# Performance work log

Measured on AMD Instinct MI355X. Metric: run time of the kernel, lower is better.

Reference implementation:

```python
import jax, jax.numpy as jnp
import numpy as np

B, T = 256, 50
N_ITEMS = 100000
EMB = 256      # embedding
KBD = 128      # KBembedding == MN_dims
HID = 256      # layers[0] == layers[-1]
OUT = 256      # out_dim
NF = 10        # MN_nfactors == n_r


def setup_inputs() -> dict:
    key = jax.random.key(0)
    ks = jax.random.split(key, 18)
    s = 0.05
    return {
        "X": jax.random.randint(ks[0], (B, T), 0, N_ITEMS),
        "E": jax.random.normal(ks[1], (N_ITEMS, EMB), jnp.float32) * s,
        "KBE": jax.random.normal(ks[2], (N_ITEMS, KBD), jnp.float32) * s,
        "r_matrix": jax.random.normal(ks[3], (NF, KBD), jnp.float32) * s,
        "W_ih": jax.random.normal(ks[4], (3 * HID, EMB), jnp.float32) * s,
        "W_hh": jax.random.normal(ks[5], (3 * HID, HID), jnp.float32) * s,
        "b_ih": jnp.zeros((3 * HID,), jnp.float32),
        "b_hh": jnp.zeros((3 * HID,), jnp.float32),
        "MNu_W": jax.random.normal(ks[6], (KBD, HID), jnp.float32) * s,
        "MNu_b": jnp.zeros((KBD,), jnp.float32),
        "MNu2_W": jax.random.normal(ks[7], (HID, KBD + HID), jnp.float32) * s,
        "MNu2_b": jnp.zeros((HID,), jnp.float32),
        "MNea_W": jax.random.normal(ks[8], (KBD, KBD), jnp.float32) * s,
        "MNea_b": jnp.zeros((KBD,), jnp.float32),
        "mlp1_W": jax.random.normal(ks[9], (OUT, HID), jnp.float32) * s,
        "mlp1_b": jnp.zeros((OUT,), jnp.float32),
        "mlp2_W": jax.random.normal(ks[10], (OUT, EMB + KBD), jnp.float32) * s,
        "mlp2_b": jnp.zeros((OUT,), jnp.float32),
    }


def _gru_cell(x, h, W_ih, W_hh, b_ih, b_hh):
    # PyTorch GRUCell: gates stacked [r, z, n] along dim 0 of weights
    gi = x @ W_ih.T + b_ih
    gh = h @ W_hh.T + b_hh
    ir, iz, inn = jnp.split(gi, 3, axis=-1)
    hr, hz, hn = jnp.split(gh, 3, axis=-1)
    r = jax.nn.sigmoid(ir + hr)
    z = jax.nn.sigmoid(iz + hz)
    n = jnp.tanh(inn + r * hn)
    return (1.0 - z) * n + z * h


def reference(X, E, KBE, r_matrix, W_ih, W_hh, b_ih, b_hh,
              MNu_W, MNu_b, MNu2_W, MNu2_b, MNea_W, MNea_b,
              mlp1_W, mlp1_b, mlp2_W, mlp2_b):
    Bv, Tv = X.shape
    Em = E.at[0].set(0.0)     # mask row 0 of E
    KBm = KBE.at[0].set(0.0)  # mask row 0 of KBE
    Sx = Em[X]                # (B, T, EMB)
    KBItem = KBm[X]           # (B, T, KBD)

    def step(carry, xs):
        h, MN, y_sum = carry
        x_t, kb_t = xs                      # (B, EMB), (B, KBD)
        h = _gru_cell(x_t, h, W_ih, W_hh, b_ih, b_hh)
        y = h                                # dropout p=0 -> identity
        # gated memory write
        EA = jnp.tanh(kb_t @ MNea_W.T + MNea_b)          # (B, KBD)
        EA = EA[:, None, :] + r_matrix                    # (B, NF, KBD)
        gate = jax.nn.sigmoid(jnp.sum(MN * EA, axis=-1, keepdims=True))  # (B, NF, 1)
        MN = MN * (1.0 - gate) + EA * gate
        # attention read
        U = jnp.tanh(y @ MNu_W.T + MNu_b)                 # (B, KBD)
        AW = jax.nn.softmax(U @ r_matrix.T, axis=1)       # (B, NF)
        AC = jnp.einsum('bfd,bf->bd', MN, AW)             # (B, KBD)
        Ut = jnp.tanh(jnp.concatenate([y, AC], axis=-1) @ MNu2_W.T + MNu2_b)  # (B, HID)
        y_out = jnp.tanh(Ut @ mlp1_W.T + mlp1_b)          # (B, OUT)
        return (h, MN, y_sum + y_out), None

    init = (jnp.zeros((Bv, HID), Sx.dtype),
            jnp.zeros((Bv, NF, KBD), Sx.dtype),
            jnp.zeros((Bv, OUT), Sx.dtype))
    xs = (jnp.swapaxes(Sx, 0, 1), jnp.swapaxes(KBItem, 0, 1))  # (T, B, *)
    (h, MN, y_sum), _ = jax.lax.scan(step, init, xs)
    y = y_sum / Tv

    MergeE = jnp.concatenate([E, KBE], axis=1).at[0].set(0.0)  # (N, EMB+KBD)
    Sy = jnp.tanh(MergeE @ mlp2_W.T + mlp2_b)                  # (N, OUT)
    scores = jax.nn.log_softmax(y @ Sy.T, axis=1)              # (B, N)
    return scores, y
```

## Files before the change

kernel.cpp:

```cpp
#include <hip/hip_runtime.h>

typedef _Float16 f16;
typedef _Float16 f16x2 __attribute__((ext_vector_type(2)));
typedef _Float16 f16x8 __attribute__((ext_vector_type(8)));
typedef float f32x4 __attribute__((ext_vector_type(4)));
typedef int i32x4 __attribute__((ext_vector_type(4)));

#define MFMA16(a,b,c) __builtin_amdgcn_mfma_f32_16x16x32_f16(a,b,c,0,0,0)

#define NITEMS 100000
#define NBLK4  1563

#define OFF_WIH   0u
#define OFF_WHH   393216u
#define OFF_MNU   786432u
#define OFF_MNU2  851968u
#define OFF_MNEA  1048576u
#define OFF_MLP1  1081344u
#define OFF_MLP2  1212416u
#define OFF_WHHD  1409024u
#define OFF_GI    1802240u
#define OFF_TV    21463040u
#define OFF_MN    24739840u
#define OFF_YALL  57507840u
#define OFF_SY    64061440u
#define OFF_Y16   115261440u
#define OFF_PMAX  115392512u
#define OFF_PSUM  117030912u
#define OFF_LSE   118669312u

__device__ __forceinline__ float sigm(float x) { return 1.f / (1.f + __expf(-x)); }
__device__ __forceinline__ float tanh_fast(float x) {
  return 1.f - 2.f / (1.f + __expf(2.f * x));
}
__device__ __forceinline__ float fdot2(f16x2 a, f16x2 b, float c) {
#if defined(__has_builtin)
#if __has_builtin(__builtin_amdgcn_fdot2)
  return __builtin_amdgcn_fdot2(a, b, c, false);
#else
  return fmaf((float)a[1], (float)b[1], fmaf((float)a[0], (float)b[0], c));
#endif
#else
  return fmaf((float)a[1], (float)b[1], fmaf((float)a[0], (float)b[0], c));
#endif
}

__global__ __launch_bounds__(256) void k_pack(
    const float* s0, const float* s1, const float* s2, const float* s3,
    const float* s4, const float* s5, const float* s6, f16* base)
{
  int fid = blockIdx.x * 256 + threadIdx.x;
  if (fid >= 88064) {
    int g = fid - 88064;
    const float* sp = s1 + (size_t)g * 8;
    f16* dst = (f16*)((char*)base + OFF_WHHD);
    f16x8 v;
    #pragma unroll
    for (int j = 0; j < 8; j++) v[j] = (f16)sp[j];
    *(f16x8*)(dst + (size_t)g * 8) = v;
    return;
  }
  const float* src; f16* dst; int K, f;
  if (fid < 24576)      { src = s0; dst = base;          K = 256; f = fid; }
  else if (fid < 49152) { src = s1; dst = base + 196608; K = 256; f = fid - 24576; }
  else if (fid < 53248) { src = s2; dst = base + 393216; K = 256; f = fid - 49152; }
  else if (fid < 65536) { src = s3; dst = base + 425984; K = 384; f = fid - 53248; }
  else if (fid < 67584) { src = s4; dst = base + 524288; K = 128; f = fid - 65536; }
  else if (fid < 75776) { src = s5; dst = base + 540672; K = 256; f = fid - 67584; }
  else                  { src = s6; dst = base + 606208; K = 384; f = fid - 75776; }
  int lane = f & 63, t2 = f >> 6, KS = K >> 5;
  int ks = t2 % KS, nt = t2 / KS;
  int row = nt * 16 + (lane & 15), col = ks * 32 + ((lane >> 4) << 3);
  const float* sp = src + (size_t)row * K + col;
  f16x8 v;
  #pragma unroll
  for (int j = 0; j < 8; j++) v[j] = (f16)sp[j];
  *(f16x8*)(dst + (size_t)f * 8) = v;
}

__global__ __launch_bounds__(512) void k_prep(
    const int* __restrict__ X, const float* __restrict__ E,
    const f16* __restrict__ Wih_p, const float* __restrict__ bih,
    const float* __restrict__ bhh, f16* __restrict__ gi,
    const float* __restrict__ KBE, const f16* __restrict__ Wea_p,
    const float* __restrict__ bea, f16* __restrict__ tv,
    const f16* __restrict__ mlp2_p, const float* __restrict__ mlp2b, f16* __restrict__ Sy)
{
  __shared__ __align__(16) char smem[66048];
  f16 (*At)[264] = (f16(*)[264])smem;
  f16* Lg2 = (f16*)(smem + 16896);
  int tid = threadIdx.x;
  int w = tid >> 6, lane = tid & 63, lr = lane & 15, lg = lane >> 4;
  if (blockIdx.x < 400) {
    int r0g = blockIdx.x * 32;
    int t = r0g >> 8;
    {
      int r = tid >> 4, c = (tid & 15) * 16;
      int b = (r0g + r) & 255;
      int item = X[b * 50 + t];
      if (item == 0) {
        #pragma unroll
        for (int j = 0; j < 16; j++) At[r][c + j] = (f16)0.f;
      } else {
        const float4* sp = (const float4*)(E + (size_t)item * 256 + c);
        #pragma unroll
        for (int q = 0; q < 4; q++) {
          float4 v = sp[q];
          At[r][c + q*4 + 0] = (f16)v.x; At[r][c + q*4 + 1] = (f16)v.y;
          At[r][c + q*4 + 2] = (f16)v.z; At[r][c + q*4 + 3] = (f16)v.w;
        }
      }
    }
    __syncthreads();
    f32x4 acc[2][6] = {};
    for (int ks = 0; ks < 8; ks++) {
      f16x8 a0 = *(const f16x8*)(&At[lr][ks * 32 + lg * 8]);
      f16x8 a1 = *(const f16x8*)(&At[16 + lr][ks * 32 + lg * 8]);
      #pragma unroll
      for (int j = 0; j < 6; j++) {
        int nt = w * 6 + j;
        f16x8 bf = *(const f16x8*)(Wih_p + ((size_t)((nt * 8 + ks) * 64 + lane) << 3));
        acc[0][j] = MFMA16(a0, bf, acc[0][j]);
        acc[1][j] = MFMA16(a1, bf, acc[1][j]);
      }
    }
    #pragma unroll
    for (int j = 0; j < 6; j++) {
      int col = (w * 6 + j) * 16 + lr;
      float bias = bih[col] + (col < 512 ? bhh[col] : 0.f);
      #pragma unroll
      for (int mt = 0; mt < 2; mt++)
        #pragma unroll
        for (int rr = 0; rr < 4; rr++)
          Lg2[(mt * 16 + lg * 4 + rr) * 768 + col] = (f16)(acc[mt][j][rr] + bias);
    }
    __syncthreads();
    f16* dst = gi + (size_t)r0g * 768;
    #pragma unroll
    for (int q = 0; q < 6; q++) {
      int u = q * 512 + tid;
      *(f16x8*)(dst + u * 8) = *(const f16x8*)(Lg2 + u * 8);
    }
  } else if (blockIdx.x < 800) {
    int r0 = (blockIdx.x - 400) * 32;
    int t = r0 >> 8;
    {
      int r = tid >> 4, c = (tid & 15) * 8;
      int b = (r0 + r) & 255;
      int item = X[b * 50 + t];
      if (item == 0) {
        #pragma unroll
        for (int j = 0; j < 8; j++) At[r][c + j] = (f16)0.f;
      } else {
        const float4* sp = (const float4*)(KBE + (size_t)item * 128 + c);
        #pragma unroll
        for (int q = 0; q < 2; q++) {
          float4 v = sp[q];
          At[r][c + q*4 + 0] = (f16)v.x; At[r][c + q*4 + 1] = (f16)v.y;
          At[r][c + q*4 + 2] = (f16)v.z; At[r][c + q*4 + 3] = (f16)v.w;
        }
      }
    }
    __syncthreads();
    f32x4 acc[2] = {};
    for (int ks = 0; ks < 4; ks++) {
      f16x8 a0 = *(const f16x8*)(&At[lr][ks * 32 + lg * 8]);
      f16x8 a1 = *(const f16x8*)(&At[16 + lr][ks * 32 + lg * 8]);
      f16x8 bf = *(const f16x8*)(Wea_p + ((size_t)((w * 4 + ks) * 64 + lane) << 3));
      acc[0] = MFMA16(a0, bf, acc[0]);
      acc[1] = MFMA16(a1, bf, acc[1]);
    }
    f16* tvs = Lg2;
    int col = w * 16 + lr;
    float bias = bea[col];
    #pragma unroll
    for (int mt = 0; mt < 2; mt++)
      #pragma unroll
      for (int rr = 0; rr < 4; rr++)
        tvs[(mt * 16 + lg * 4 + rr) * 128 + col] = (f16)tanh_fast(acc[mt][rr] + bias);
    __syncthreads();
    {
      int row = tid >> 4, c = (tid & 15) * 8;
      *(f16x8*)(tv + (size_t)(r0 + row) * 128 + c) = *(const f16x8*)(tvs + row * 128 + c);
    }
  } else {
    f16* A2 = (f16*)smem;
    int i0 = (blockIdx.x - 800) * 32;
    {
      int r = tid >> 4;
      int item = i0 + r;
      f16* rowp = A2 + r * 392;
      int cE = (tid & 15) * 16, cK = (tid & 15) * 8;
      if (item == 0) {
        #pragma unroll
        for (int j = 0; j < 16; j++) rowp[cE + j] = (f16)0.f;
        #pragma unroll
        for (int j = 0; j < 8; j++) rowp[256 + cK + j] = (f16)0.f;
      } else {
        const float4* sp = (const float4*)(E + (size_t)item * 256 + cE);
        #pragma unroll
        for (int q = 0; q < 4; q++) {
          float4 v = sp[q];
          rowp[cE + q*4 + 0] = (f16)v.x; rowp[cE + q*4 + 1] = (f16)v.y;
          rowp[cE + q*4 + 2] = (f16)v.z; rowp[cE + q*4 + 3] = (f16)v.w;
        }
        const float4* kp = (const float4*)(KBE + (size_t)item * 128 + cK);
        #pragma unroll
        for (int q = 0; q < 2; q++) {
          float4 v = kp[q];
          rowp[256 + cK + q*4 + 0] = (f16)v.x; rowp[256 + cK + q*4 + 1] = (f16)v.y;
          rowp[256 + cK + q*4 + 2] = (f16)v.z; rowp[256 + cK + q*4 + 3] = (f16)v.w;
        }
      }
    }
    __syncthreads();
    int mt = w & 1, nq = w >> 1;
    f32x4 acc[4] = {};
    for (int ks = 0; ks < 12; ks++) {
      f16x8 a = *(const f16x8*)(&A2[(mt * 16 + lr) * 392 + ks * 32 + lg * 8]);
      #pragma unroll
      for (int j = 0; j < 4; j++) {
        int nt = nq * 4 + j;
        f16x8 bf = *(const f16x8*)(mlp2_p + ((size_t)((nt * 12 + ks) * 64 + lane) << 3));
        acc[j] = MFMA16(a, bf, acc[j]);
      }
    }
    #pragma unroll
    for (int j = 0; j < 4; j++) {
      int col = (nq * 4 + j) * 16 + lr;
      float bias = mlp2b[col];
      #pragma unroll
      for (int rr = 0; rr < 4; rr++) {
        int item = i0 + mt * 16 + lg * 4 + rr;
        Sy[(size_t)item * 256 + col] = (f16)tanh_fast(acc[j][rr] + bias);
      }
    }
  }
}

__global__ __launch_bounds__(1024) void k_scan(
    const f16* __restrict__ Whh_d, const float* __restrict__ bhh,
    const f16* __restrict__ gi, f16* __restrict__ y_all,
    const f16* __restrict__ tv, const float* __restrict__ Rm, f16* __restrict__ MN)
{
  int tid = threadIdx.x, w = tid >> 6, l = tid & 63;
  if (blockIdx.x < 256) {
    __shared__ __align__(16) f16 hbuf[4 * 72];
    __shared__ float ghbuf[768];
    int b = blockIdx.x;
    int chunk = l >> 4, cl = l & 15;
    i32x4 Wv[3][8];
    #pragma unroll
    for (int j = 0; j < 3; j++) {
      int col = w * 48 + j * 16 + cl;
      const f16* wp = Whh_d + (size_t)col * 256 + chunk * 64;
      #pragma unroll
      for (int m = 0; m < 8; m++)
        Wv[j][m] = *(const i32x4*)(wp + m * 8);
    }
    float hprev = 0.f, bN = 0.f;
    f16 gr = (f16)0.f, gz = (f16)0.f, gn = (f16)0.f;
    if (tid < 256) {
      hbuf[(tid >> 6) * 72 + (tid & 63)] = (f16)0.f;
      bN = bhh[512 + tid];
      const f16* g0 = gi + (size_t)b * 768 + tid;
      gr = g0[0]; gz = g0[256]; gn = g0[512];
    }
    __syncthreads();
    const f16* hb = hbuf + chunk * 72;
    for (int t = 0; t < 50; t++) {
      float s0 = 0.f, s1 = 0.f, s2 = 0.f;
      #pragma unroll
      for (int m = 0; m < 8; m++) {
        i32x4 hw = *(const i32x4*)(hb + m * 8);
        #pragma unroll
        for (int p = 0; p < 4; p++) {
          f16x2 hp = __builtin_bit_cast(f16x2, hw[p]);
          s0 = fdot2(hp, __builtin_bit_cast(f16x2, Wv[0][m][p]), s0);
          s1 = fdot2(hp, __builtin_bit_cast(f16x2, Wv[1][m][p]), s1);
          s2 = fdot2(hp, __builtin_bit_cast(f16x2, Wv[2][m][p]), s2);
        }
      }
      s0 += __shfl_xor(s0, 16); s0 += __shfl_xor(s0, 32);
      s1 += __shfl_xor(s1, 16); s1 += __shfl_xor(s1, 32);
      s2 += __shfl_xor(s2, 16); s2 += __shfl_xor(s2, 32);
      if (l < 16) {
        ghbuf[w * 48 + l]      = s0;
        ghbuf[w * 48 + 16 + l] = s1;
        ghbuf[w * 48 + 32 + l] = s2;
      }
      __syncthreads();
      if (tid < 256) {
        int c = tid;
        float rg = sigm((float)gr + ghbuf[c]);
        float zg = sigm((float)gz + ghbuf[256 + c]);
        float ng = tanh_fast((float)gn + rg * (ghbuf[512 + c] + bN));
        float hv = ng + zg * (hprev - ng);
        hprev = hv;
        hbuf[(c >> 6) * 72 + (c & 63)] = (f16)hv;
        y_all[((size_t)t * 256 + b) * 256 + c] = (f16)hv;
        if (t < 49) {
          const f16* gN = gi + ((size_t)(t + 1) * 256 + b) * 768 + c;
          gr = gN[0]; gz = gN[256]; gn = gN[512];
        }
      }
      __syncthreads();
    }
  } else {
    int lane = l;
    int pair = (blockIdx.x - 256) * 16 + w;
    int b = pair / 10, f = pair - (pair / 10) * 10;
    float r0_ = Rm[f * 128 + lane], r1_ = Rm[f * 128 + 64 + lane];
    float mn0 = 0.f, mn1 = 0.f;
    float c0 = (float)tv[(size_t)b * 128 + lane];
    float c1 = (float)tv[(size_t)b * 128 + 64 + lane];
    for (int t = 0; t < 50; t++) {
      float ea0 = c0 + r0_;
      float ea1 = c1 + r1_;
      if (t < 49) {
        size_t nb = ((size_t)(t + 1) * 256 + b) * 128;
        c0 = (float)tv[nb + lane];
        c1 = (float)tv[nb + 64 + lane];
      }
      float p = mn0 * ea0 + mn1 * ea1;
      #pragma unroll
      for (int off = 32; off > 0; off >>= 1) p += __shfl_xor(p, off);
      float g = sigm(p);
      mn0 += (ea0 - mn0) * g;
      mn1 += (ea1 - mn1) * g;
      size_t mb = (((size_t)t * 256 + b) * 10 + f) * 128;
      MN[mb + lane] = (f16)mn0;
      MN[mb + 64 + lane] = (f16)mn1;
    }
  }
}

__global__ __launch_bounds__(512) void k_uacut(
    const f16* __restrict__ y_all, const f16* __restrict__ MNu_p,
    const float* __restrict__ MNub, const float* __restrict__ Rm,
    const f16* __restrict__ MN,
    const f16* __restrict__ MNu2_p, const float* __restrict__ MNu2b,
    const f16* __restrict__ mlp1_p, const float* __restrict__ mlp1b,
    float* __restrict__ ypart)
{
  __shared__ __align__(16) char smem[25088];
  int tid = threadIdx.x, w = tid >> 6, lane = tid & 63, lr = lane & 15, lg = lane >> 4;
  f16   (*Aty)[264] = (f16(*)[264])smem;
  float (*Uf)[136]  = (float(*)[136])(smem + 8448);
  f16   (*Utl)[264] = (f16(*)[264])(smem + 8448);
  float (*Lg)[10]   = (float(*)[10])(smem + 17152);
  float (*Aw)[10]   = (float(*)[10])(smem + 17792);
  f16   (*ACs)[136] = (f16(*)[136])(smem + 18432);
  int r0 = blockIdx.x * 16;
  {
    int r = tid >> 5, c = (tid & 31) * 8;
    f16x8 v = *(const f16x8*)(y_all + (size_t)(r0 + r) * 256 + c);
    *(f16x8*)(&Aty[r][c]) = v;
  }
  __syncthreads();
  {
    f32x4 acc = {};
    for (int ks = 0; ks < 8; ks++) {
      f16x8 a = *(const f16x8*)(&Aty[lr][ks * 32 + lg * 8]);
      f16x8 bf = *(const f16x8*)(MNu_p + ((size_t)((w * 8 + ks) * 64 + lane) << 3));
      acc = MFMA16(a, bf, acc);
    }
    int col = w * 16 + lr;
    float bias = MNub[col];
    #pragma unroll
    for (int rr = 0; rr < 4; rr++)
      Uf[lg * 4 + rr][col] = tanh_fast(acc[rr] + bias);
  }
  __syncthreads();
  if (tid < 160) {
    int row = tid / 10, f = tid - (tid / 10) * 10;
    float s = 0.f;
    for (int d = 0; d < 128; d++) s += Uf[row][d] * Rm[f * 128 + d];
    Lg[row][f] = s;
  }
  __syncthreads();
  if (tid < 16) {
    float m = -1e30f;
    #pragma unroll
    for (int f = 0; f < 10; f++) m = fmaxf(m, Lg[tid][f]);
    float e[10], s = 0.f;
    #pragma unroll
    for (int f = 0; f < 10; f++) { e[f] = __expf(Lg[tid][f] - m); s += e[f]; }
    float inv = 1.f / s;
    #pragma unroll
    for (int f = 0; f < 10; f++) Aw[tid][f] = e[f] * inv;
  }
  __syncthreads();
  if (tid < 256) {
    int row = tid >> 4, d0 = (tid & 15) * 8;
    float a[8] = {0,0,0,0,0,0,0,0};
    for (int f = 0; f < 10; f++) {
      float wgt = Aw[row][f];
      f16x8 mv = *(const f16x8*)(MN + (((size_t)(r0 + row)) * 10 + f) * 128 + d0);
      #pragma unroll
      for (int q = 0; q < 8; q++) a[q] += wgt * (float)mv[q];
    }
    f16x8 o;
    #pragma unroll
    for (int q = 0; q < 8; q++) o[q] = (f16)a[q];
    *(f16x8*)(&ACs[row][d0]) = o;
  }
  __syncthreads();
  {
    f32x4 acc[2] = {};
    for (int ks = 0; ks < 12; ks++) {
      f16x8 a = (ks < 8)
        ? *(const f16x8*)(&Aty[lr][ks * 32 + lg * 8])
        : *(const f16x8*)(&ACs[lr][(ks - 8) * 32 + lg * 8]);
      #pragma unroll
      for (int j = 0; j < 2; j++) {
        f16x8 bf = *(const f16x8*)(MNu2_p + ((size_t)(((w * 2 + j) * 12 + ks) * 64 + lane) << 3));
        acc[j] = MFMA16(a, bf, acc[j]);
      }
    }
    __syncthreads();
    #pragma unroll
    for (int j = 0; j < 2; j++) {
      int col = (w * 2 + j) * 16 + lr;
      float bias = MNu2b[col];
      #pragma unroll
      for (int rr = 0; rr < 4; rr++)
        Utl[lg * 4 + rr][col] = (f16)tanh_fast(acc[j][rr] + bias);
    }
  }
  __syncthreads();
  {
    f32x4 acc2[2] = {};
    for (int ks = 0; ks < 8; ks++) {
      f16x8 a = *(const f16x8*)(&Utl[lr][ks * 32 + lg * 8]);
      #pragma unroll
      for (int j = 0; j < 2; j++) {
        f16x8 bf = *(const f16x8*)(mlp1_p + ((size_t)(((w * 2 + j) * 8 + ks) * 64 + lane) << 3));
        acc2[j] = MFMA16(a, bf, acc2[j]);
      }
    }
    #pragma unroll
    for (int j = 0; j < 2; j++) {
      int col = (w * 2 + j) * 16 + lr;
      float bias = mlp1b[col];
      #pragma unroll
      for (int rr = 0; rr < 4; rr++) {
        int row = r0 + lg * 4 + rr;
        ypart[(size_t)row * 256 + col] = tanh_fast(acc2[j][rr] + bias);
      }
    }
  }
}

__global__ __launch_bounds__(256) void k_yfin(
    const float* __restrict__ ypart, float* __restrict__ outy, f16* __restrict__ y16)
{
  int b = blockIdx.x, c = threadIdx.x;
  float s = 0.f;
  for (int t = 0; t < 50; t++) s += ypart[((size_t)t * 256 + b) * 256 + c];
  float v = s * (1.0f / 50.0f);
  outy[b * 256 + c] = v;
  y16[b * 256 + c] = (f16)v;
}

__global__ __launch_bounds__(512) void k_score0(
    const f16* __restrict__ y16, const f16* __restrict__ Sy,
    float* __restrict__ pmax, float* __restrict__ psum)
{
  __shared__ float pm[512], ps[512];
  int tid = threadIdx.x, w = tid >> 6, lane = tid & 63, lr = lane & 15, lg = lane >> 4;
  int i0 = blockIdx.x * 64;
  int mtb = (w >> 1) * 4, ntb = (w & 1) * 2;
  f32x4 acc[4][2] = {};
  for (int ks = 0; ks < 8; ks++) {
    f16x8 a[4];
    #pragma unroll
    for (int i = 0; i < 4; i++)
      a[i] = *(const f16x8*)(y16 + ((size_t)((mtb + i) * 16 + lr)) * 256 + ks * 32 + lg * 8);
    #pragma unroll
    for (int j = 0; j < 2; j++) {
      int item = i0 + (ntb + j) * 16 + lr;
      int ic = item < NITEMS ? item : (NITEMS - 1);
      f16x8 bv = *(const f16x8*)(Sy + (size_t)ic * 256 + ks * 32 + lg * 8);
      #pragma unroll
      for (int i = 0; i < 4; i++) acc[i][j] = MFMA16(a[i], bv, acc[i][j]);
    }
  }
  {
    int item0 = i0 + ntb * 16 + lr, item1 = item0 + 16;
    bool v0 = item0 < NITEMS, v1 = item1 < NITEMS;
    #pragma unroll
    for (int i = 0; i < 4; i++)
      #pragma unroll
      for (int rr = 0; rr < 4; rr++) {
        float x0 = v0 ? acc[i][0][rr] : -1e30f;
        float x1 = v1 ? acc[i][1][rr] : -1e30f;
        float m = fmaxf(x0, x1);
        m = fmaxf(m, __shfl_xor(m, 1)); m = fmaxf(m, __shfl_xor(m, 2));
        m = fmaxf(m, __shfl_xor(m, 4)); m = fmaxf(m, __shfl_xor(m, 8));
        float s = (v0 ? __expf(x0 - m) : 0.f) + (v1 ? __expf(x1 - m) : 0.f);
        s += __shfl_xor(s, 1); s += __shfl_xor(s, 2);
        s += __shfl_xor(s, 4); s += __shfl_xor(s, 8);
        if (lr == 0) {
          int row = (mtb + i) * 16 + lg * 4 + rr;
          pm[(w & 1) * 256 + row] = m;
          ps[(w & 1) * 256 + row] = s;
        }
      }
  }
  __syncthreads();
  if (tid < 256) {
    float m0 = pm[tid], m1 = pm[256 + tid];
    float s0 = ps[tid], s1 = ps[256 + tid];
    float M = fmaxf(m0, m1);
    float S = s0 * __expf(m0 - M) + s1 * __expf(m1 - M);
    pmax[(size_t)tid * 1600 + blockIdx.x] = M;
    psum[(size_t)tid * 1600 + blockIdx.x] = S;
  }
}

__global__ __launch_bounds__(256) void k_lse(
    const float* __restrict__ pmax, const float* __restrict__ psum, float* __restrict__ lse)
{
  int b = blockIdx.x, tid = threadIdx.x;
  __shared__ float red[256];
  float m = -1e30f;
  for (int i = tid; i < NBLK4; i += 256) m = fmaxf(m, pmax[(size_t)b * 1600 + i]);
  red[tid] = m; __syncthreads();
  for (int s = 128; s > 0; s >>= 1) {
    if (tid < s) red[tid] = fmaxf(red[tid], red[tid + s]);
    __syncthreads();
  }
  float M = red[0]; __syncthreads();
  float s = 0.f;
  for (int i = tid; i < NBLK4; i += 256)
    s += psum[(size_t)b * 1600 + i] * __expf(pmax[(size_t)b * 1600 + i] - M);
  red[tid] = s; __syncthreads();
  for (int q = 128; q > 0; q >>= 1) {
    if (tid < q) red[tid] += red[tid + q];
    __syncthreads();
  }
  if (tid == 0) lse[b] = M + logf(red[0]);
}

__global__ __launch_bounds__(512) void k_scores1(
    const f16* __restrict__ y16, const f16* __restrict__ Sy,
    const float* __restrict__ lse, float* __restrict__ out)
{
  __shared__ float lse_s[256];
  int tid = threadIdx.x, w = tid >> 6, lane = tid & 63, lr = lane & 15, lg = lane >> 4;
  if (tid < 256) lse_s[tid] = lse[tid];
  int i0 = blockIdx.x * 64;
  int mtb = (w >> 1) * 4, ntb = (w & 1) * 2;
  f32x4 acc[4][2] = {};
  for (int ks = 0; ks < 8; ks++) {
    f16x8 a[4];
    #pragma unroll
    for (int i = 0; i < 4; i++)
      a[i] = *(const f16x8*)(y16 + ((size_t)((mtb + i) * 16 + lr)) * 256 + ks * 32 + lg * 8);
    #pragma unroll
    for (int j = 0; j < 2; j++) {
      int item = i0 + (ntb + j) * 16 + lr;
      int ic = item < NITEMS ? item : (NITEMS - 1);
      f16x8 bv = *(const f16x8*)(Sy + (size_t)ic * 256 + ks * 32 + lg * 8);
      #pragma unroll
      for (int i = 0; i < 4; i++) acc[i][j] = MFMA16(a[i], bv, acc[i][j]);
    }
  }
  __syncthreads();
  #pragma unroll
  for (int i = 0; i < 4; i++)
    #pragma unroll
    for (int j = 0; j < 2; j++) {
      int c = i0 + (ntb + j) * 16 + lr;
      if (c < NITEMS) {
        #pragma unroll
        for (int rr = 0; rr < 4; rr++) {
          int row = (mtb + i) * 16 + lg * 4 + rr;
          out[(size_t)row * NITEMS + c] = acc[i][j][rr] - lse_s[row];
        }
      }
    }
}

extern "C" void kernel_launch(void* const* d_in, const int* in_sizes, int n_in,
                              void* d_out, int out_size, void* d_ws, size_t ws_size,
                              hipStream_t stream) {
  (void)in_sizes; (void)n_in; (void)out_size; (void)ws_size;
  const int*   X     = (const int*)d_in[0];
  const float* E     = (const float*)d_in[1];
  const float* KBE   = (const float*)d_in[2];
  const float* Rm    = (const float*)d_in[3];
  const float* Wih   = (const float*)d_in[4];
  const float* Whh   = (const float*)d_in[5];
  const float* bih   = (const float*)d_in[6];
  const float* bhh   = (const float*)d_in[7];
  const float* MNuW  = (const float*)d_in[8];
  const float* MNub  = (const float*)d_in[9];
  const float* MNu2W = (const float*)d_in[10];
  const float* MNu2b = (const float*)d_in[11];
  const float* MNeaW = (const float*)d_in[12];
  const float* MNeab = (const float*)d_in[13];
  const float* mlp1W = (const float*)d_in[14];
  const float* mlp1b = (const float*)d_in[15];
  const float* mlp2W = (const float*)d_in[16];
  const float* mlp2b = (const float*)d_in[17];

  char* ws = (char*)d_ws;
  f16*   Wih_p  = (f16*)(ws + OFF_WIH);
  f16*   MNu_p  = (f16*)(ws + OFF_MNU);
  f16*   MNu2_p = (f16*)(ws + OFF_MNU2);
  f16*   Wea_p  = (f16*)(ws + OFF_MNEA);
  f16*   mlp1_p = (f16*)(ws + OFF_MLP1);
  f16*   mlp2_p = (f16*)(ws + OFF_MLP2);
  f16*   Whh_d  = (f16*)(ws + OFF_WHHD);
  f16*   gi     = (f16*)(ws + OFF_GI);
  f16*   tv     = (f16*)(ws + OFF_TV);
  f16*   MN     = (f16*)(ws + OFF_MN);
  f16*   y_all  = (f16*)(ws + OFF_YALL);
  f16*   Sy     = (f16*)(ws + OFF_SY);
  float* ypart  = (float*)(ws + OFF_GI);
  f16*   y16    = (f16*)(ws + OFF_Y16);
  float* pmax   = (float*)(ws + OFF_PMAX);
  float* psum   = (float*)(ws + OFF_PSUM);
  float* lse    = (float*)(ws + OFF_LSE);
  float* outf   = (float*)d_out;

  k_pack<<<440, 256, 0, stream>>>(Wih, Whh, MNuW, MNu2W, MNeaW, mlp1W, mlp2W, (f16*)ws);
  k_prep<<<3925, 512, 0, stream>>>(X, E, Wih_p, bih, bhh, gi, KBE, Wea_p, MNeab, tv,
                                   mlp2_p, mlp2b, Sy);
  k_scan<<<416, 1024, 0, stream>>>(Whh_d, bhh, gi, y_all, tv, Rm, MN);
  k_uacut<<<800, 512, 0, stream>>>(y_all, MNu_p, MNub, Rm, MN,
                                   MNu2_p, MNu2b, mlp1_p, mlp1b, ypart);
  k_yfin<<<256, 256, 0, stream>>>(ypart, outf + 25600000, y16);
  k_score0<<<NBLK4, 512, 0, stream>>>(y16, Sy, pmax, psum);
  k_lse<<<256, 256, 0, stream>>>(pmax, psum, lse);
  k_scores1<<<NBLK4, 512, 0, stream>>>(y16, Sy, lse, outf);
}
```

Measured before the change: 398.6 us.

## Move item projection (Sy) into the scan kernel to overlap with the recurrence

The Sy = tanh(MergeE @ mlp2_W.T) computation over all 100k items moves out of the prep kernel and into extra blocks of the scan launch, rewritten for 1024-thread blocks. The 256 serial GRU blocks and 160 memory-network blocks run alongside 3125 independent GEMM blocks, so the latency-bound recurrence can be hidden behind the bandwidth-heavy item projection. The risk is that the GEMM blocks compete with the latency-critical scan blocks for CU resources. The scan blocks also hit the launch_bounds(1024) register limit while holding weights in registers.

```diff
diff --git a/kernel.cpp b/kernel.cpp
--- a/kernel.cpp
+++ b/kernel.cpp
@@ -83,8 +83,7 @@
     const f16* __restrict__ Wih_p, const float* __restrict__ bih,
     const float* __restrict__ bhh, f16* __restrict__ gi,
     const float* __restrict__ KBE, const f16* __restrict__ Wea_p,
-    const float* __restrict__ bea, f16* __restrict__ tv,
-    const f16* __restrict__ mlp2_p, const float* __restrict__ mlp2b, f16* __restrict__ Sy)
+    const float* __restrict__ bea, f16* __restrict__ tv)
 {
   __shared__ __align__(16) char smem[66048];
   f16 (*At)[264] = (f16(*)[264])smem;
@@ -141,7 +140,7 @@
       int u = q * 512 + tid;
       *(f16x8*)(dst + u * 8) = *(const f16x8*)(Lg2 + u * 8);
     }
-  } else if (blockIdx.x < 800) {
+  } else {
     int r0 = (blockIdx.x - 400) * 32;
     int t = r0 >> 8;
     {
@@ -183,70 +182,21 @@
       int row = tid >> 4, c = (tid & 15) * 8;
       *(f16x8*)(tv + (size_t)(r0 + row) * 128 + c) = *(const f16x8*)(tvs + row * 128 + c);
     }
-  } else {
-    f16* A2 = (f16*)smem;
-    int i0 = (blockIdx.x - 800) * 32;
-    {
-      int r = tid >> 4;
-      int item = i0 + r;
-      f16* rowp = A2 + r * 392;
-      int cE = (tid & 15) * 16, cK = (tid & 15) * 8;
-      if (item == 0) {
-        #pragma unroll
-        for (int j = 0; j < 16; j++) rowp[cE + j] = (f16)0.f;
-        #pragma unroll
-        for (int j = 0; j < 8; j++) rowp[256 + cK + j] = (f16)0.f;
-      } else {
-        const float4* sp = (const float4*)(E + (size_t)item * 256 + cE);
-        #pragma unroll
-        for (int q = 0; q < 4; q++) {
-          float4 v = sp[q];
-          rowp[cE + q*4 + 0] = (f16)v.x; rowp[cE + q*4 + 1] = (f16)v.y;
-          rowp[cE + q*4 + 2] = (f16)v.z; rowp[cE + q*4 + 3] = (f16)v.w;
-        }
-        const float4* kp = (const float4*)(KBE + (size_t)item * 128 + cK);
-        #pragma unroll
-        for (int q = 0; q < 2; q++) {
-          float4 v = kp[q];
-          rowp[256 + cK + q*4 + 0] = (f16)v.x; rowp[256 + cK + q*4 + 1] = (f16)v.y;
-          rowp[256 + cK + q*4 + 2] = (f16)v.z; rowp[256 + cK + q*4 + 3] = (f16)v.w;
-        }
-      }
-    }
-    __syncthreads();
-    int mt = w & 1, nq = w >> 1;
-    f32x4 acc[4] = {};
-    for (int ks = 0; ks < 12; ks++) {
-      f16x8 a = *(const f16x8*)(&A2[(mt * 16 + lr) * 392 + ks * 32 + lg * 8]);
-      #pragma unroll
-      for (int j = 0; j < 4; j++) {
-        int nt = nq * 4 + j;
-        f16x8 bf = *(const f16x8*)(mlp2_p + ((size_t)((nt * 12 + ks) * 64 + lane) << 3));
-        acc[j] = MFMA16(a, bf, acc[j]);
-      }
-    }
-    #pragma unroll
-    for (int j = 0; j < 4; j++) {
-      int col = (nq * 4 + j) * 16 + lr;
-      float bias = mlp2b[col];
-      #pragma unroll
-      for (int rr = 0; rr < 4; rr++) {
-        int item = i0 + mt * 16 + lg * 4 + rr;
-        Sy[(size_t)item * 256 + col] = (f16)tanh_fast(acc[j][rr] + bias);
-      }
-    }
-  }
-}
-
-__global__ __launch_bounds__(1024) void k_scan(
+  }
+}
+
+__global__ __launch_bounds__(1024) void k_fused2(
     const f16* __restrict__ Whh_d, const float* __restrict__ bhh,
     const f16* __restrict__ gi, f16* __restrict__ y_all,
-    const f16* __restrict__ tv, const float* __restrict__ Rm, f16* __restrict__ MN)
-{
+    const f16* __restrict__ tv, const float* __restrict__ Rm, f16* __restrict__ MN,
+    const float* __restrict__ E, const float* __restrict__ KBE,
+    const f16* __restrict__ mlp2_p, const float* __restrict__ mlp2b, f16* __restrict__ Sy)
+{
+  __shared__ __align__(16) char smem[25088];
   int tid = threadIdx.x, w = tid >> 6, l = tid & 63;
   if (blockIdx.x < 256) {
-    __shared__ __align__(16) f16 hbuf[4 * 72];
-    __shared__ float ghbuf[768];
+    f16* hbuf = (f16*)smem;
+    float* ghbuf = (float*)(smem + 1024);
     int b = blockIdx.x;
     int chunk = l >> 4, cl = l & 15;
     i32x4 Wv[3][8];
@@ -306,7 +256,7 @@
       }
       __syncthreads();
     }
-  } else {
+  } else if (blockIdx.x < 416) {
     int lane = l;
     int pair = (blockIdx.x - 256) * 16 + w;
     int b = pair / 10, f = pair - (pair / 10) * 10;
@@ -331,6 +281,58 @@
       size_t mb = (((size_t)t * 256 + b) * 10 + f) * 128;
       MN[mb + lane] = (f16)mn0;
       MN[mb + 64 + lane] = (f16)mn1;
+    }
+  } else {
+    f16* At = (f16*)smem;
+    int lane = l, lr = lane & 15, lg = lane >> 4;
+    int i0 = (blockIdx.x - 416) * 32;
+    {
+      int r = tid >> 5;
+      int item = i0 + r;
+      int c = (tid & 31) * 8;
+      if (item == 0) {
+        #pragma unroll
+        for (int j = 0; j < 8; j++) At[r * 392 + c + j] = (f16)0.f;
+      } else {
+        const float4* sp = (const float4*)(E + (size_t)item * 256 + c);
+        #pragma unroll
+        for (int q = 0; q < 2; q++) {
+          float4 v = sp[q];
+          At[r * 392 + c + q*4 + 0] = (f16)v.x; At[r * 392 + c + q*4 + 1] = (f16)v.y;
+          At[r * 392 + c + q*4 + 2] = (f16)v.z; At[r * 392 + c + q*4 + 3] = (f16)v.w;
+        }
+      }
+      int c2 = (tid & 31) * 4;
+      if (item == 0) {
+        #pragma unroll
+        for (int j = 0; j < 4; j++) At[r * 392 + 256 + c2 + j] = (f16)0.f;
+      } else {
+        float4 v = *(const float4*)(KBE + (size_t)item * 128 + c2);
+        At[r * 392 + 256 + c2 + 0] = (f16)v.x; At[r * 392 + 256 + c2 + 1] = (f16)v.y;
+        At[r * 392 + 256 + c2 + 2] = (f16)v.z; At[r * 392 + 256 + c2 + 3] = (f16)v.w;
+      }
+    }
+    __syncthreads();
+    int mt = w & 1, ntp = w >> 1;
+    f32x4 acc[2] = {};
+    for (int ks = 0; ks < 12; ks++) {
+      f16x8 a = *(const f16x8*)(&At[(mt * 16 + lr) * 392 + ks * 32 + lg * 8]);
+      #pragma unroll
+      for (int j = 0; j < 2; j++) {
+        int nt = ntp * 2 + j;
+        f16x8 bf = *(const f16x8*)(mlp2_p + ((size_t)((nt * 12 + ks) * 64 + lane) << 3));
+        acc[j] = MFMA16(a, bf, acc[j]);
+      }
+    }
+    #pragma unroll
+    for (int j = 0; j < 2; j++) {
+      int col = (ntp * 2 + j) * 16 + lr;
+      float bias = mlp2b[col];
+      #pragma unroll
+      for (int rr = 0; rr < 4; rr++) {
+        int item = i0 + mt * 16 + lg * 4 + rr;
+        Sy[(size_t)item * 256 + col] = (f16)tanh_fast(acc[j][rr] + bias);
+      }
     }
   }
 }
@@ -627,9 +629,9 @@
   float* outf   = (float*)d_out;
 
   k_pack<<<440, 256, 0, stream>>>(Wih, Whh, MNuW, MNu2W, MNeaW, mlp1W, mlp2W, (f16*)ws);
-  k_prep<<<3925, 512, 0, stream>>>(X, E, Wih_p, bih, bhh, gi, KBE, Wea_p, MNeab, tv,
-                                   mlp2_p, mlp2b, Sy);
-  k_scan<<<416, 1024, 0, stream>>>(Whh_d, bhh, gi, y_all, tv, Rm, MN);
+  k_prep<<<800, 512, 0, stream>>>(X, E, Wih_p, bih, bhh, gi, KBE, Wea_p, MNeab, tv);
+  k_fused2<<<3541, 1024, 0, stream>>>(Whh_d, bhh, gi, y_all, tv, Rm, MN,
+                                      E, KBE, mlp2_p, mlp2b, Sy);
   k_uacut<<<800, 512, 0, stream>>>(y_all, MNu_p, MNub, Rm, MN,
                                    MNu2_p, MNu2b, mlp1_p, mlp1b, ypart);
   k_yfin<<<256, 256, 0, stream>>>(ypart, outf + 25600000, y16);
```

New measurement: 391.0 us. No clear change (-1.9%).
